# Performance work log

Hardware: AMD Instinct MI355X
Metric: run time of the kernel (lower is better)

## Reference

```python
import jax, jax.numpy as jnp
from jax import lax
import numpy as np


def conv4d(x, w, b, pad):
    """4D conv (stride 1) as a sum of 3D convs over the first-spatial-dim kernel taps.
    x: [B, Cin, T, D, H, W]; w: [Cout, Cin, Kt, Kd, Kh, Kw]; same pad on all dims."""
    B, Cin, T, D, H, W = x.shape
    Cout, _, Kt = w.shape[:3]
    xp = jnp.pad(x, ((0, 0), (0, 0), (pad, pad), (0, 0), (0, 0), (0, 0)))
    Tout = T + 2 * pad - Kt + 1
    acc = None
    for k in range(Kt):  # loop over kernel taps (<=3), not data dims
        xs = xp[:, :, k:k + Tout]                      # [B,Cin,Tout,D,H,W]
        xs = xs.transpose(0, 2, 1, 3, 4, 5).reshape(B * Tout, Cin, D, H, W)
        y = lax.conv_general_dilated(
            xs, w[:, :, k], (1, 1, 1), [(pad, pad)] * 3,
            dimension_numbers=('NCDHW', 'OIDHW', 'NCDHW'))
        acc = y if acc is None else acc + y
    Do, Ho, Wo = acc.shape[2:]
    out = acc.reshape(B, Tout, Cout, Do, Ho, Wo).transpose(0, 2, 1, 3, 4, 5)
    return out + b[None, :, None, None, None, None]


def tconv4d_k2s2(x, w, b):
    """4D transposed conv, kernel=2, stride=2, pad=0 (non-overlapping blocks).
    x: [B,Cin,T,D,H,W]; w: [Cin,Cout,2,2,2,2] (PyTorch ConvTranspose layout)."""
    B, Cin, T, D, H, W = x.shape
    Cout = w.shape[1]
    y = jnp.einsum('bcijkl,copqrs->boipjqkrls', x, w)
    y = y.reshape(B, Cout, 2 * T, 2 * D, 2 * H, 2 * W)
    return y + b[None, :, None, None, None, None]


def setup_inputs() -> dict:
    key = jax.random.key(0)
    ks = jax.random.split(key, 10)
    Cin, Cout = 64, 32
    x1 = jax.random.normal(ks[0], (2, Cin, 8, 8, 8, 8), dtype=jnp.float32)
    x2 = jax.random.normal(ks[1], (2, Cin // 2, 16, 16, 16, 16), dtype=jnp.float32)
    def w(k, shape, fan_in):
        return jax.random.normal(k, shape, dtype=jnp.float32) / np.float32(np.sqrt(fan_in))
    up_w = w(ks[2], (Cin, Cin // 2, 2, 2, 2, 2), Cin * 16)
    up_b = w(ks[3], (Cin // 2,), Cin * 16)
    w1 = w(ks[4], (Cout, Cin, 3, 3, 3, 3), Cin * 81)
    b1 = w(ks[5], (Cout,), Cin * 81)
    w2 = w(ks[6], (Cout, Cout, 3, 3, 3, 3), Cout * 81)
    b2 = w(ks[7], (Cout,), Cout * 81)
    w3 = w(ks[8], (Cout, Cin, 1, 1, 1, 1), Cin)
    b3 = w(ks[9], (Cout,), Cin)
    return {'x1': x1, 'x2': x2, 'up_w': up_w, 'up_b': up_b,
            'w1': w1, 'b1': b1, 'w2': w2, 'b2': b2, 'w3': w3, 'b3': b3}


def reference(x1, x2, up_w, up_b, w1, b1, w2, b2, w3, b3):
    x1u = tconv4d_k2s2(x1, up_w, up_b)              # [B, Cin//2, 16,16,16,16]
    xc = jnp.concatenate([x2, x1u], axis=1)          # [B, Cin, 16,16,16,16]
    Y = jax.nn.relu(conv4d(xc, w1, b1, 1))
    Y = conv4d(Y, w2, b2, 1)
    sc = conv4d(xc, w3, b3, 0)                       # 1x1 residual projection
    return jax.nn.relu(Y + sc)
```

## Files before the change

### kernel.cpp

```cpp
#include <hip/hip_runtime.h>

typedef unsigned short u16;
typedef __attribute__((ext_vector_type(8))) short short8;
typedef __attribute__((ext_vector_type(4))) float f32x4;

#define XCB_OFF  0
#define Y1B_OFF  8388608
#define W1P_OFF  12582912
#define W2P_OFF  12748800
#define W3P_OFF  12831744
#define UPWP_OFF 12833792
#define X1T_OFF  12866560

__device__ __forceinline__ u16 f2bf(float v) {
    unsigned u = __builtin_bit_cast(unsigned, v);
    u += 0x7FFFu + ((u >> 16) & 1u);
    return (u16)(u >> 16);
}

__device__ __forceinline__ f32x4 MFMA(short8 a, short8 b, f32x4 c) {
    return __builtin_amdgcn_mfma_f32_16x16x32_bf16(a, b, c, 0, 0, 0);
}

__device__ __forceinline__ void decode_bid(int bid, int& b, int& t, int& d, int& h0) {
    int xcd = bid & 7, loc = bid >> 3;
    int hB = loc & 1;
    d = (loc >> 1) & 15;
    int tsub = (loc >> 5) & 1;
    b = loc >> 6;
    t = xcd * 2 + tsub;
    h0 = hB * 8;
}

__global__ __launch_bounds__(256) void setup(const float* __restrict__ w1,
                                             const float* __restrict__ w2,
                                             const float* __restrict__ w3,
                                             const float* __restrict__ upw,
                                             const float* __restrict__ x1,
                                             const float* __restrict__ x2,
                                             u16* __restrict__ ws) {
    __shared__ u16 lds[256 * 72];
    int bid = blockIdx.x;
    int tid = threadIdx.x;
    if (bid < 32) {
        int b = bid >> 4;
        int pos_base = (bid & 15) * 256;
        u16* x1t = ws + X1T_OFF;
        #pragma unroll
        for (int c = 0; c < 64; ++c) {
            lds[tid * 72 + c] = f2bf(x1[((b * 64 + c) << 12) + pos_base + tid]);
        }
        __syncthreads();
        #pragma unroll
        for (int k = 0; k < 8; ++k) {
            int f = k * 256 + tid;
            int u = f & 7, pos = f >> 3;
            uint4 v = *(const uint4*)(lds + pos * 72 + u * 8);
            *(uint4*)(x1t + (size_t)((b << 12) + pos_base + pos) * 64 + u * 8) = v;
        }
    } else if (bid < 544) {
        int lb = bid - 32;
        int b = lb >> 8;
        int pos_base = (lb & 255) * 256;
        u16* xcb = ws + XCB_OFF;
        #pragma unroll
        for (int c = 0; c < 32; ++c) {
            lds[tid * 40 + c] = f2bf(x2[((b * 32 + c) << 16) + pos_base + tid]);
        }
        __syncthreads();
        #pragma unroll
        for (int k = 0; k < 4; ++k) {
            int f = k * 256 + tid;
            int u = f & 3, pos = f >> 2;
            uint4 v = *(const uint4*)(lds + pos * 40 + u * 8);
            *(uint4*)(xcb + (size_t)((b << 16) + pos_base + pos) * 64 + u * 8) = v;
        }
    } else {
        int idx = (bid - 544) * 256 + tid;
        if (idx < 165888) {
            int j = idx & 7, lane = (idx >> 3) & 63, rest = idx >> 9;
            int half = rest & 1, chunk = (rest >> 1) & 1, tap = rest >> 2;
            int co = half * 16 + (lane & 15), ci = chunk * 32 + (lane >> 4) * 8 + j;
            ws[W1P_OFF + idx] = f2bf(w1[(co * 64 + ci) * 81 + tap]);
        } else if (idx < 165888 + 82944) {
            int i2 = idx - 165888;
            int j = i2 & 7, lane = (i2 >> 3) & 63, rest = i2 >> 9;
            int half = rest & 1, tap = rest >> 1;
            int co = half * 16 + (lane & 15), ci = (lane >> 4) * 8 + j;
            ws[W2P_OFF + i2] = f2bf(w2[(co * 32 + ci) * 81 + tap]);
        } else if (idx < 165888 + 82944 + 2048) {
            int i3 = idx - (165888 + 82944);
            int j = i3 & 7, lane = (i3 >> 3) & 63, rest = i3 >> 9;
            int half = rest & 1, chunk = rest >> 1;
            int co = half * 16 + (lane & 15), ci = chunk * 32 + (lane >> 4) * 8 + j;
            ws[W3P_OFF + i3] = f2bf(w3[co * 64 + ci]);
        } else if (idx < 250880 + 32768) {
            int i4 = idx - 250880;
            int j = i4 & 7, lane = (i4 >> 3) & 63, rest = i4 >> 9;
            int half = rest & 1, chunk = (rest >> 1) & 1, tap = rest >> 2;
            int co = half * 16 + (lane & 15), ci = chunk * 32 + (lane >> 4) * 8 + j;
            ws[UPWP_OFF + i4] = f2bf(upw[(ci * 32 + co) * 16 + tap]);
        }
    }
}

__global__ __launch_bounds__(256) void xc_up_mfma(const u16* __restrict__ x1t,
                                                  const u16* __restrict__ upwp,
                                                  const float* __restrict__ up_b,
                                                  u16* __restrict__ xcb) {
    int tid = threadIdx.x;
    int wv = tid >> 6, lane = tid & 63;
    int q = lane >> 4, m = lane & 15;
    int wid = blockIdx.x * 4 + wv;
    int j = wid & 63, tap = (wid >> 6) & 15, b = wid >> 10;

    f32x4 acc[4][2];
    {
        float4 bi0 = ((const float4*)up_b)[q];
        float4 bi1 = ((const float4*)up_b)[4 + q];
        #pragma unroll
        for (int g = 0; g < 4; ++g) {
            acc[g][0] = (f32x4){bi0.x, bi0.y, bi0.z, bi0.w};
            acc[g][1] = (f32x4){bi1.x, bi1.y, bi1.z, bi1.w};
        }
    }

    const short8* wv8 = (const short8*)upwp;
    const u16* xb = x1t + (size_t)((b << 12) + (j << 6) + m) * 64;
    #pragma unroll
    for (int chunk = 0; chunk < 2; ++chunk) {
        short8 a0 = wv8[((tap * 2 + chunk) * 2 + 0) * 64 + lane];
        short8 a1 = wv8[((tap * 2 + chunk) * 2 + 1) * 64 + lane];
        #pragma unroll
        for (int g = 0; g < 4; ++g) {
            short8 bf = *(const short8*)(xb + (size_t)(g * 16) * 64 + chunk * 32 + q * 8);
            acc[g][0] = MFMA(a0, bf, acc[g][0]);
            acc[g][1] = MFMA(a1, bf, acc[g][1]);
        }
    }

    int it = j >> 3, id = j & 7;
    int pt = tap >> 3, pd = (tap >> 2) & 1, ph = (tap >> 1) & 1, pw = tap & 1;
    int oT = 2 * it + pt, oD = 2 * id + pd, oW = 2 * (m & 7) + pw;
    #pragma unroll
    for (int g = 0; g < 4; ++g) {
        int ih = g * 2 + (m >> 3);
        int opos = oT * 4096 + oD * 256 + (2 * ih + ph) * 16 + oW;
        u16* op = xcb + (size_t)((b << 16) + opos) * 64 + 32 + q * 4;
        #pragma unroll
        for (int half = 0; half < 2; ++half) {
            f32x4 v = acc[g][half];
            uint2 o;
            o.x = (unsigned)f2bf(v.x) | ((unsigned)f2bf(v.y) << 16);
            o.y = (unsigned)f2bf(v.z) | ((unsigned)f2bf(v.w) << 16);
            *(uint2*)(op + half * 16) = o;
        }
    }
}

__global__ __launch_bounds__(256, 4) void conv1_mfma(const u16* __restrict__ xcb,
                                                     const u16* __restrict__ w1p,
                                                     const float* __restrict__ b1,
                                                     u16* __restrict__ y1b) {
    __shared__ u16 lds[11520];
    int tid = threadIdx.x;
    int lane = tid & 63, wv = tid >> 6;
    int q = lane >> 4, m = lane & 15;
    int c = wv & 1, rg = wv >> 1;
    int b, t, d, h0;
    decode_bid(blockIdx.x, b, t, d, h0);
    int rot = (blockIdx.x * 5) % 9;

    int lofs[6], gofs[6];
    bool st[6], inr[6];
    #pragma unroll
    for (int k = 0; k < 6; ++k) {
        int ui = tid + k * 256;
        int u = ui & 7, p = (ui >> 3) % 18, hh = ui / 144;
        int gh = h0 - 1 + hh, gw = p - 1;
        st[k] = ui < 1440;
        inr[k] = st[k] && ((unsigned)gh < 16u) && ((unsigned)gw < 16u);
        gofs[k] = (gh * 16 + gw) * 64 + u * 8;
        lofs[k] = hh * 1152 + p * 64 + ((u ^ (p & 7)) * 8);
    }

    f32x4 acc[4][2];
    if (c == 0) {
        float4 bi0 = ((const float4*)b1)[q];
        float4 bi1 = ((const float4*)b1)[4 + q];
        #pragma unroll
        for (int i = 0; i < 4; ++i) {
            acc[i][0] = (f32x4){bi0.x, bi0.y, bi0.z, bi0.w};
            acc[i][1] = (f32x4){bi1.x, bi1.y, bi1.z, bi1.w};
        }
    } else {
        #pragma unroll
        for (int i = 0; i < 4; ++i) {
            acc[i][0] = (f32x4){0.f, 0.f, 0.f, 0.f};
            acc[i][1] = (f32x4){0.f, 0.f, 0.f, 0.f};
        }
    }
    const short8* w1v = (const short8*)w1p;

    uint4 rP[6];
    auto load_plane = [&](int ktd) {
        int kt = ktd / 3, kd = ktd - kt * 3;
        int tt = t + kt - 1, dd = d + kd - 1;
        bool pv = ((unsigned)tt < 16u) && ((unsigned)dd < 16u);
        const u16* src = xcb + (size_t)(((b * 16 + tt) * 16 + dd)) * 16384;
        #pragma unroll
        for (int k = 0; k < 6; ++k) {
            uint4 v = {0, 0, 0, 0};
            if (pv && inr[k]) v = *(const uint4*)(src + gofs[k]);
            rP[k] = v;
        }
    };
    auto write_plane = [&]() {
        #pragma unroll
        for (int k = 0; k < 6; ++k)
            if (st[k]) *(uint4*)(lds + lofs[k]) = rP[k];
    };

    load_plane(rot);
    for (int s = 0; s < 9; ++s) {
        int ktd = rot + s; if (ktd >= 9) ktd -= 9;
        __syncthreads();
        write_plane();
        if (s < 8) {
            int nk = ktd + 1; if (nk >= 9) nk -= 9;
            load_plane(nk);
        }
        __syncthreads();
        __builtin_amdgcn_s_setprio(1);
        #pragma unroll
        for (int kw = 0; kw < 3; ++kw) {
            int p = kw + m, pm = p & 7;
            int bo = p * 64 + ((((c << 2) | q) ^ pm) << 3);
            short8 R[6];
            #pragma unroll
            for (int r = 0; r < 6; ++r)
                R[r] = *(const short8*)(lds + (rg * 4 + r) * 1152 + bo);
            #pragma unroll
            for (int kh = 0; kh < 3; ++kh) {
                int tap = (ktd * 3 + kh) * 3 + kw;
                short8 a0 = w1v[((tap * 2 + c) * 2 + 0) * 64 + lane];
                short8 a1 = w1v[((tap * 2 + c) * 2 + 1) * 64 + lane];
                #pragma unroll
                for (int i = 0; i < 4; ++i) {
                    acc[i][0] = MFMA(a0, R[i + kh], acc[i][0]);
                    acc[i][1] = MFMA(a1, R[i + kh], acc[i][1]);
                }
            }
        }
        __builtin_amdgcn_s_setprio(0);
    }

    __syncthreads();
    f32x4* buf = (f32x4*)lds;
    if (c == 1) {
        #pragma unroll
        for (int i = 0; i < 4; ++i)
            #pragma unroll
            for (int half = 0; half < 2; ++half)
                buf[((rg * 4 + i) * 2 + half) * 64 + lane] = acc[i][half];
    }
    __syncthreads();
    if (c == 0) {
        int obase = ((b * 16 + t) * 16 + d) * 256 + (h0 + rg * 4) * 16 + m;
        #pragma unroll
        for (int i = 0; i < 4; ++i) {
            int pos = obase + i * 16;
            #pragma unroll
            for (int half = 0; half < 2; ++half) {
                f32x4 v = acc[i][half];
                f32x4 w = buf[((rg * 4 + i) * 2 + half) * 64 + lane];
                v.x += w.x; v.y += w.y; v.z += w.z; v.w += w.w;
                unsigned r0 = f2bf(fmaxf(v.x, 0.f)), r1 = f2bf(fmaxf(v.y, 0.f));
                unsigned r2 = f2bf(fmaxf(v.z, 0.f)), r3 = f2bf(fmaxf(v.w, 0.f));
                uint2 o;
                o.x = r0 | (r1 << 16);
                o.y = r2 | (r3 << 16);
                *(uint2*)(y1b + (size_t)pos * 32 + half * 16 + q * 4) = o;
            }
        }
    }
}

__global__ __launch_bounds__(256, 4) void conv2_mfma(const u16* __restrict__ y1b,
                                                     const u16* __restrict__ xcb,
                                                     const u16* __restrict__ w2p,
                                                     const u16* __restrict__ w3p,
                                                     const float* __restrict__ b2,
                                                     const float* __restrict__ b3,
                                                     float* __restrict__ out) {
    __shared__ u16 lds[2][5760];
    int tid = threadIdx.x;
    int lane = tid & 63, wv = tid >> 6;
    int q = lane >> 4, m = lane & 15;
    int hf = wv & 1, rg = wv >> 1;
    int b, t, d, h0;
    decode_bid(blockIdx.x, b, t, d, h0);
    int rot = (blockIdx.x * 5) % 9;

    int lofs[3], gofs[3];
    bool st[3], inr[3];
    #pragma unroll
    for (int k = 0; k < 3; ++k) {
        int ui = tid + k * 256;
        int u = ui & 3, p = (ui >> 2) % 18, hh = ui / 72;
        int gh = h0 - 1 + hh, gw = p - 1;
        st[k] = ui < 720;
        inr[k] = st[k] && ((unsigned)gh < 16u) && ((unsigned)gw < 16u);
        gofs[k] = (gh * 16 + gw) * 32 + u * 8;
        lofs[k] = hh * 576 + p * 32 + ((u ^ (p & 3)) * 8);
    }

    f32x4 acc[4];
    {
        float4 p0 = ((const float4*)b2)[hf * 4 + q];
        float4 s0 = ((const float4*)b3)[hf * 4 + q];
        #pragma unroll
        for (int i = 0; i < 4; ++i)
            acc[i] = (f32x4){p0.x + s0.x, p0.y + s0.y, p0.z + s0.z, p0.w + s0.w};
    }
    const short8* w2v = (const short8*)w2p;

    uint4 rP[3];
    auto load_plane = [&](int ktd) {
        int kt = ktd / 3, kd = ktd - kt * 3;
        int tt = t + kt - 1, dd = d + kd - 1;
        bool pv = ((unsigned)tt < 16u) && ((unsigned)dd < 16u);
        const u16* src = y1b + (size_t)(((b * 16 + tt) * 16 + dd)) * 8192;
        #pragma unroll
        for (int k = 0; k < 3; ++k) {
            uint4 v = {0, 0, 0, 0};
            if (pv && inr[k]) v = *(const uint4*)(src + gofs[k]);
            rP[k] = v;
        }
    };
    auto write_plane = [&](int bb) {
        #pragma unroll
        for (int k = 0; k < 3; ++k)
            if (st[k]) *(uint4*)(&lds[bb][lofs[k]]) = rP[k];
    };

    load_plane(rot);
    write_plane(0);
    { int nk = rot + 1; if (nk >= 9) nk -= 9; load_plane(nk); }

    for (int s = 0; s < 9; ++s) {
        int ktd = rot + s; if (ktd >= 9) ktd -= 9;
        __syncthreads();
        const u16* L = lds[s & 1];
        __builtin_amdgcn_s_setprio(1);
        #pragma unroll
        for (int kw = 0; kw < 3; ++kw) {
            int p = kw + m, pm = p & 3;
            int bo = p * 32 + ((q ^ pm) << 3);
            short8 R[6];
            #pragma unroll
            for (int r = 0; r < 6; ++r)
                R[r] = *(const short8*)(L + (rg * 4 + r) * 576 + bo);
            #pragma unroll
            for (int kh = 0; kh < 3; ++kh) {
                int tap = (ktd * 3 + kh) * 3 + kw;
                short8 a = w2v[(tap * 2 + hf) * 64 + lane];
                #pragma unroll
                for (int i = 0; i < 4; ++i) {
                    acc[i] = MFMA(a, R[i + kh], acc[i]);
                }
            }
        }
        __builtin_amdgcn_s_setprio(0);
        if (s < 8) {
            write_plane((s + 1) & 1);
            if (s < 7) {
                int nk = ktd + 2; if (nk >= 9) nk -= 9;
                load_plane(nk);
            }
        }
    }

    const short8* w3v = (const short8*)w3p;
    int lpos0 = (t * 16 + d) * 256 + (h0 + rg * 4) * 16 + m;
    int gpos0 = (b << 16) + lpos0;
    #pragma unroll
    for (int chunk = 0; chunk < 2; ++chunk) {
        short8 a = w3v[(chunk * 2 + hf) * 64 + lane];
        #pragma unroll
        for (int i = 0; i < 4; ++i) {
            short8 bf = *(const short8*)(xcb + (size_t)(gpos0 + i * 16) * 64 + ((chunk << 2) | q) * 8);
            acc[i] = MFMA(a, bf, acc[i]);
        }
    }

    #pragma unroll
    for (int i = 0; i < 4; ++i) {
        int lpos = lpos0 + i * 16;
        f32x4 v = acc[i];
        int co = hf * 16 + q * 4;
        float* op = out + (((size_t)(b * 32 + co)) << 16) + lpos;
        op[0ull << 16] = fmaxf(v.x, 0.f);
        op[1ull << 16] = fmaxf(v.y, 0.f);
        op[2ull << 16] = fmaxf(v.z, 0.f);
        op[3ull << 16] = fmaxf(v.w, 0.f);
    }
}

extern "C" void kernel_launch(void* const* d_in, const int* in_sizes, int n_in,
                              void* d_out, int out_size, void* d_ws, size_t ws_size,
                              hipStream_t stream) {
    const float* x1   = (const float*)d_in[0];
    const float* x2   = (const float*)d_in[1];
    const float* up_w = (const float*)d_in[2];
    const float* up_b = (const float*)d_in[3];
    const float* w1   = (const float*)d_in[4];
    const float* b1   = (const float*)d_in[5];
    const float* w2   = (const float*)d_in[6];
    const float* b2   = (const float*)d_in[7];
    const float* w3   = (const float*)d_in[8];
    const float* b3   = (const float*)d_in[9];
    u16* ws  = (u16*)d_ws;
    float* out = (float*)d_out;

    setup<<<1652, 256, 0, stream>>>(w1, w2, w3, up_w, x1, x2, ws);
    xc_up_mfma<<<512, 256, 0, stream>>>(ws + X1T_OFF, ws + UPWP_OFF, up_b, ws + XCB_OFF);
    conv1_mfma<<<1024, 256, 0, stream>>>(ws + XCB_OFF, ws + W1P_OFF, b1, ws + Y1B_OFF);
    conv2_mfma<<<1024, 256, 0, stream>>>(ws + Y1B_OFF, ws + XCB_OFF, ws + W2P_OFF,
                                         ws + W3P_OFF, b2, b3, out);
}
```

Before: 159.6 us.

## Give each conv2 block a full H plane and all 32 output channels

```diff
diff --git a/kernel.cpp b/kernel.cpp
--- a/kernel.cpp
+++ b/kernel.cpp
@@ -286,53 +286,60 @@
     }
 }
 
-__global__ __launch_bounds__(256, 4) void conv2_mfma(const u16* __restrict__ y1b,
+__global__ __launch_bounds__(256, 2) void conv2_mfma(const u16* __restrict__ y1b,
                                                      const u16* __restrict__ xcb,
                                                      const u16* __restrict__ w2p,
                                                      const u16* __restrict__ w3p,
                                                      const float* __restrict__ b2,
                                                      const float* __restrict__ b3,
                                                      float* __restrict__ out) {
-    __shared__ u16 lds[2][5760];
+    __shared__ u16 lds[2][10368];
     int tid = threadIdx.x;
     int lane = tid & 63, wv = tid >> 6;
     int q = lane >> 4, m = lane & 15;
-    int hf = wv & 1, rg = wv >> 1;
-    int b, t, d, h0;
-    decode_bid(blockIdx.x, b, t, d, h0);
-    int rot = (blockIdx.x * 5) % 9;
-
-    int lofs[3], gofs[3];
-    bool st[3], inr[3];
-    #pragma unroll
-    for (int k = 0; k < 3; ++k) {
+    int rg = wv;
+    int bid = blockIdx.x;
+    int xcd = bid & 7, loc = bid >> 3;
+    int d = loc & 15;
+    int tsub = (loc >> 4) & 1;
+    int b = loc >> 5;
+    int t = xcd * 2 + tsub;
+    int rot = (bid * 5) % 9;
+
+    int lofs[6], gofs[6];
+    bool st[6], inr[6];
+    #pragma unroll
+    for (int k = 0; k < 6; ++k) {
         int ui = tid + k * 256;
         int u = ui & 3, p = (ui >> 2) % 18, hh = ui / 72;
-        int gh = h0 - 1 + hh, gw = p - 1;
-        st[k] = ui < 720;
+        int gh = hh - 1, gw = p - 1;
+        st[k] = ui < 1296;
         inr[k] = st[k] && ((unsigned)gh < 16u) && ((unsigned)gw < 16u);
         gofs[k] = (gh * 16 + gw) * 32 + u * 8;
         lofs[k] = hh * 576 + p * 32 + ((u ^ (p & 3)) * 8);
     }
 
-    f32x4 acc[4];
+    f32x4 acc[4][2];
     {
-        float4 p0 = ((const float4*)b2)[hf * 4 + q];
-        float4 s0 = ((const float4*)b3)[hf * 4 + q];
-        #pragma unroll
-        for (int i = 0; i < 4; ++i)
-            acc[i] = (f32x4){p0.x + s0.x, p0.y + s0.y, p0.z + s0.z, p0.w + s0.w};
+        #pragma unroll
+        for (int hf = 0; hf < 2; ++hf) {
+            float4 p0 = ((const float4*)b2)[hf * 4 + q];
+            float4 s0 = ((const float4*)b3)[hf * 4 + q];
+            #pragma unroll
+            for (int i = 0; i < 4; ++i)
+                acc[i][hf] = (f32x4){p0.x + s0.x, p0.y + s0.y, p0.z + s0.z, p0.w + s0.w};
+        }
     }
     const short8* w2v = (const short8*)w2p;
 
-    uint4 rP[3];
+    uint4 rP[6];
     auto load_plane = [&](int ktd) {
         int kt = ktd / 3, kd = ktd - kt * 3;
         int tt = t + kt - 1, dd = d + kd - 1;
         bool pv = ((unsigned)tt < 16u) && ((unsigned)dd < 16u);
         const u16* src = y1b + (size_t)(((b * 16 + tt) * 16 + dd)) * 8192;
         #pragma unroll
-        for (int k = 0; k < 3; ++k) {
+        for (int k = 0; k < 6; ++k) {
             uint4 v = {0, 0, 0, 0};
             if (pv && inr[k]) v = *(const uint4*)(src + gofs[k]);
             rP[k] = v;
@@ -340,7 +347,7 @@
     };
     auto write_plane = [&](int bb) {
         #pragma unroll
-        for (int k = 0; k < 3; ++k)
+        for (int k = 0; k < 6; ++k)
             if (st[k]) *(uint4*)(&lds[bb][lofs[k]]) = rP[k];
     };
 
@@ -364,10 +371,12 @@
             #pragma unroll
             for (int kh = 0; kh < 3; ++kh) {
                 int tap = (ktd * 3 + kh) * 3 + kw;
-                short8 a = w2v[(tap * 2 + hf) * 64 + lane];
+                short8 a0 = w2v[(tap * 2 + 0) * 64 + lane];
+                short8 a1 = w2v[(tap * 2 + 1) * 64 + lane];
                 #pragma unroll
                 for (int i = 0; i < 4; ++i) {
-                    acc[i] = MFMA(a, R[i + kh], acc[i]);
+                    acc[i][0] = MFMA(a0, R[i + kh], acc[i][0]);
+                    acc[i][1] = MFMA(a1, R[i + kh], acc[i][1]);
                 }
             }
         }
@@ -382,28 +391,33 @@
     }
 
     const short8* w3v = (const short8*)w3p;
-    int lpos0 = (t * 16 + d) * 256 + (h0 + rg * 4) * 16 + m;
+    int lpos0 = (t * 16 + d) * 256 + (rg * 4) * 16 + m;
     int gpos0 = (b << 16) + lpos0;
     #pragma unroll
     for (int chunk = 0; chunk < 2; ++chunk) {
-        short8 a = w3v[(chunk * 2 + hf) * 64 + lane];
+        short8 a0 = w3v[(chunk * 2 + 0) * 64 + lane];
+        short8 a1 = w3v[(chunk * 2 + 1) * 64 + lane];
         #pragma unroll
         for (int i = 0; i < 4; ++i) {
             short8 bf = *(const short8*)(xcb + (size_t)(gpos0 + i * 16) * 64 + ((chunk << 2) | q) * 8);
-            acc[i] = MFMA(a, bf, acc[i]);
+            acc[i][0] = MFMA(a0, bf, acc[i][0]);
+            acc[i][1] = MFMA(a1, bf, acc[i][1]);
         }
     }
 
     #pragma unroll
     for (int i = 0; i < 4; ++i) {
         int lpos = lpos0 + i * 16;
-        f32x4 v = acc[i];
-        int co = hf * 16 + q * 4;
-        float* op = out + (((size_t)(b * 32 + co)) << 16) + lpos;
-        op[0ull << 16] = fmaxf(v.x, 0.f);
-        op[1ull << 16] = fmaxf(v.y, 0.f);
-        op[2ull << 16] = fmaxf(v.z, 0.f);
-        op[3ull << 16] = fmaxf(v.w, 0.f);
+        #pragma unroll
+        for (int hf = 0; hf < 2; ++hf) {
+            f32x4 v = acc[i][hf];
+            int co = hf * 16 + q * 4;
+            float* op = out + (((size_t)(b * 32 + co)) << 16) + lpos;
+            op[0ull << 16] = fmaxf(v.x, 0.f);
+            op[1ull << 16] = fmaxf(v.y, 0.f);
+            op[2ull << 16] = fmaxf(v.z, 0.f);
+            op[3ull << 16] = fmaxf(v.w, 0.f);
+        }
     }
 }
 
@@ -426,6 +440,6 @@
     setup<<<1652, 256, 0, stream>>>(w1, w2, w3, up_w, x1, x2, ws);
     xc_up_mfma<<<512, 256, 0, stream>>>(ws + X1T_OFF, ws + UPWP_OFF, up_b, ws + XCB_OFF);
     conv1_mfma<<<1024, 256, 0, stream>>>(ws + XCB_OFF, ws + W1P_OFF, b1, ws + Y1B_OFF);
-    conv2_mfma<<<1024, 256, 0, stream>>>(ws + Y1B_OFF, ws + XCB_OFF, ws + W2P_OFF,
-                                         ws + W3P_OFF, b2, b3, out);
-}
+    conv2_mfma<<<512, 256, 0, stream>>>(ws + Y1B_OFF, ws + XCB_OFF, ws + W2P_OFF,
+                                        ws + W3P_OFF, b2, b3, out);
+}
```

Result: no change. 159.1 us (-0.3%).

## Fuse x1 bf16 transpose into upsample kernel and re-tile conv2 warps

Applied to the files above, without the earlier changes.

```diff
diff --git a/kernel.cpp b/kernel.cpp
--- a/kernel.cpp
+++ b/kernel.cpp
@@ -10,7 +10,6 @@
 #define W2P_OFF  12748800
 #define W3P_OFF  12831744
 #define UPWP_OFF 12833792
-#define X1T_OFF  12866560
 
 __device__ __forceinline__ u16 f2bf(float v) {
     unsigned u = __builtin_bit_cast(unsigned, v);
@@ -36,32 +35,14 @@
                                              const float* __restrict__ w2,
                                              const float* __restrict__ w3,
                                              const float* __restrict__ upw,
-                                             const float* __restrict__ x1,
                                              const float* __restrict__ x2,
                                              u16* __restrict__ ws) {
-    __shared__ u16 lds[256 * 72];
+    __shared__ u16 lds[256 * 40];
     int bid = blockIdx.x;
     int tid = threadIdx.x;
-    if (bid < 32) {
-        int b = bid >> 4;
-        int pos_base = (bid & 15) * 256;
-        u16* x1t = ws + X1T_OFF;
-        #pragma unroll
-        for (int c = 0; c < 64; ++c) {
-            lds[tid * 72 + c] = f2bf(x1[((b * 64 + c) << 12) + pos_base + tid]);
-        }
-        __syncthreads();
-        #pragma unroll
-        for (int k = 0; k < 8; ++k) {
-            int f = k * 256 + tid;
-            int u = f & 7, pos = f >> 3;
-            uint4 v = *(const uint4*)(lds + pos * 72 + u * 8);
-            *(uint4*)(x1t + (size_t)((b << 12) + pos_base + pos) * 64 + u * 8) = v;
-        }
-    } else if (bid < 544) {
-        int lb = bid - 32;
-        int b = lb >> 8;
-        int pos_base = (lb & 255) * 256;
+    if (bid < 512) {
+        int b = bid >> 8;
+        int pos_base = (bid & 255) * 256;
         u16* xcb = ws + XCB_OFF;
         #pragma unroll
         for (int c = 0; c < 32; ++c) {
@@ -76,7 +57,7 @@
             *(uint4*)(xcb + (size_t)((b << 16) + pos_base + pos) * 64 + u * 8) = v;
         }
     } else {
-        int idx = (bid - 544) * 256 + tid;
+        int idx = (bid - 512) * 256 + tid;
         if (idx < 165888) {
             int j = idx & 7, lane = (idx >> 3) & 63, rest = idx >> 9;
             int half = rest & 1, chunk = (rest >> 1) & 1, tap = rest >> 2;
@@ -104,56 +85,64 @@
     }
 }
 
-__global__ __launch_bounds__(256) void xc_up_mfma(const u16* __restrict__ x1t,
+__global__ __launch_bounds__(256) void xc_up_mfma(const float* __restrict__ x1,
                                                   const u16* __restrict__ upwp,
                                                   const float* __restrict__ up_b,
                                                   u16* __restrict__ xcb) {
+    __shared__ u16 lds[64 * 72];
     int tid = threadIdx.x;
     int wv = tid >> 6, lane = tid & 63;
     int q = lane >> 4, m = lane & 15;
-    int wid = blockIdx.x * 4 + wv;
-    int j = wid & 63, tap = (wid >> 6) & 15, b = wid >> 10;
-
-    f32x4 acc[4][2];
-    {
-        float4 bi0 = ((const float4*)up_b)[q];
-        float4 bi1 = ((const float4*)up_b)[4 + q];
+    int bid = blockIdx.x;
+    int j = bid & 63, b = bid >> 6;
+    int pos_base = j * 64;
+
+    #pragma unroll
+    for (int g = 0; g < 16; ++g) {
+        int c = g * 4 + wv;
+        lds[lane * 72 + c] = f2bf(x1[((b * 64 + c) << 12) + pos_base + lane]);
+    }
+    __syncthreads();
+
+    const short8* wv8 = (const short8*)upwp;
+    float4 bi0 = ((const float4*)up_b)[q];
+    float4 bi1 = ((const float4*)up_b)[4 + q];
+    int it = j >> 3, id = j & 7;
+
+    for (int tt = 0; tt < 4; ++tt) {
+        int tap = wv * 4 + tt;
+        f32x4 acc[4][2];
         #pragma unroll
         for (int g = 0; g < 4; ++g) {
             acc[g][0] = (f32x4){bi0.x, bi0.y, bi0.z, bi0.w};
             acc[g][1] = (f32x4){bi1.x, bi1.y, bi1.z, bi1.w};
         }
-    }
-
-    const short8* wv8 = (const short8*)upwp;
-    const u16* xb = x1t + (size_t)((b << 12) + (j << 6) + m) * 64;
-    #pragma unroll
-    for (int chunk = 0; chunk < 2; ++chunk) {
-        short8 a0 = wv8[((tap * 2 + chunk) * 2 + 0) * 64 + lane];
-        short8 a1 = wv8[((tap * 2 + chunk) * 2 + 1) * 64 + lane];
+        #pragma unroll
+        for (int chunk = 0; chunk < 2; ++chunk) {
+            short8 a0 = wv8[((tap * 2 + chunk) * 2 + 0) * 64 + lane];
+            short8 a1 = wv8[((tap * 2 + chunk) * 2 + 1) * 64 + lane];
+            #pragma unroll
+            for (int g = 0; g < 4; ++g) {
+                short8 bf = *(const short8*)(lds + (g * 16 + m) * 72 + chunk * 32 + q * 8);
+                acc[g][0] = MFMA(a0, bf, acc[g][0]);
+                acc[g][1] = MFMA(a1, bf, acc[g][1]);
+            }
+        }
+        int pt = tap >> 3, pd = (tap >> 2) & 1, ph = (tap >> 1) & 1, pw = tap & 1;
+        int oT = 2 * it + pt, oD = 2 * id + pd, oW = 2 * (m & 7) + pw;
         #pragma unroll
         for (int g = 0; g < 4; ++g) {
-            short8 bf = *(const short8*)(xb + (size_t)(g * 16) * 64 + chunk * 32 + q * 8);
-            acc[g][0] = MFMA(a0, bf, acc[g][0]);
-            acc[g][1] = MFMA(a1, bf, acc[g][1]);
-        }
-    }
-
-    int it = j >> 3, id = j & 7;
-    int pt = tap >> 3, pd = (tap >> 2) & 1, ph = (tap >> 1) & 1, pw = tap & 1;
-    int oT = 2 * it + pt, oD = 2 * id + pd, oW = 2 * (m & 7) + pw;
-    #pragma unroll
-    for (int g = 0; g < 4; ++g) {
-        int ih = g * 2 + (m >> 3);
-        int opos = oT * 4096 + oD * 256 + (2 * ih + ph) * 16 + oW;
-        u16* op = xcb + (size_t)((b << 16) + opos) * 64 + 32 + q * 4;
-        #pragma unroll
-        for (int half = 0; half < 2; ++half) {
-            f32x4 v = acc[g][half];
-            uint2 o;
-            o.x = (unsigned)f2bf(v.x) | ((unsigned)f2bf(v.y) << 16);
-            o.y = (unsigned)f2bf(v.z) | ((unsigned)f2bf(v.w) << 16);
-            *(uint2*)(op + half * 16) = o;
+            int ih = g * 2 + (m >> 3);
+            int opos = oT * 4096 + oD * 256 + (2 * ih + ph) * 16 + oW;
+            u16* op = xcb + (size_t)((b << 16) + opos) * 64 + 32 + q * 4;
+            #pragma unroll
+            for (int half = 0; half < 2; ++half) {
+                f32x4 v = acc[g][half];
+                uint2 o;
+                o.x = (unsigned)f2bf(v.x) | ((unsigned)f2bf(v.y) << 16);
+                o.y = (unsigned)f2bf(v.z) | ((unsigned)f2bf(v.w) << 16);
+                *(uint2*)(op + half * 16) = o;
+            }
         }
     }
 }
@@ -293,11 +282,11 @@
                                                      const float* __restrict__ b2,
                                                      const float* __restrict__ b3,
                                                      float* __restrict__ out) {
-    __shared__ u16 lds[2][5760];
+    __shared__ u16 lds[11520];
     int tid = threadIdx.x;
     int lane = tid & 63, wv = tid >> 6;
     int q = lane >> 4, m = lane & 15;
-    int hf = wv & 1, rg = wv >> 1;
+    int rg = wv;
     int b, t, d, h0;
     decode_bid(blockIdx.x, b, t, d, h0);
     int rot = (blockIdx.x * 5) % 9;
@@ -315,13 +304,14 @@
         lofs[k] = hh * 576 + p * 32 + ((u ^ (p & 3)) * 8);
     }
 
-    f32x4 acc[4];
-    {
+    f32x4 acc[2][2];
+    #pragma unroll
+    for (int hf = 0; hf < 2; ++hf) {
         float4 p0 = ((const float4*)b2)[hf * 4 + q];
         float4 s0 = ((const float4*)b3)[hf * 4 + q];
         #pragma unroll
-        for (int i = 0; i < 4; ++i)
-            acc[i] = (f32x4){p0.x + s0.x, p0.y + s0.y, p0.z + s0.z, p0.w + s0.w};
+        for (int i = 0; i < 2; ++i)
+            acc[i][hf] = (f32x4){p0.x + s0.x, p0.y + s0.y, p0.z + s0.z, p0.w + s0.w};
     }
     const short8* w2v = (const short8*)w2p;
 
@@ -341,7 +331,7 @@
     auto write_plane = [&](int bb) {
         #pragma unroll
         for (int k = 0; k < 3; ++k)
-            if (st[k]) *(uint4*)(&lds[bb][lofs[k]]) = rP[k];
+            if (st[k]) *(uint4*)(lds + bb * 5760 + lofs[k]) = rP[k];
     };
 
     load_plane(rot);
@@ -351,23 +341,25 @@
     for (int s = 0; s < 9; ++s) {
         int ktd = rot + s; if (ktd >= 9) ktd -= 9;
         __syncthreads();
-        const u16* L = lds[s & 1];
+        const u16* L = lds + (s & 1) * 5760;
         __builtin_amdgcn_s_setprio(1);
         #pragma unroll
         for (int kw = 0; kw < 3; ++kw) {
             int p = kw + m, pm = p & 3;
             int bo = p * 32 + ((q ^ pm) << 3);
-            short8 R[6];
-            #pragma unroll
-            for (int r = 0; r < 6; ++r)
-                R[r] = *(const short8*)(L + (rg * 4 + r) * 576 + bo);
+            short8 R[4];
+            #pragma unroll
+            for (int r = 0; r < 4; ++r)
+                R[r] = *(const short8*)(L + (rg * 2 + r) * 576 + bo);
             #pragma unroll
             for (int kh = 0; kh < 3; ++kh) {
                 int tap = (ktd * 3 + kh) * 3 + kw;
-                short8 a = w2v[(tap * 2 + hf) * 64 + lane];
+                short8 a0 = w2v[(tap * 2 + 0) * 64 + lane];
+                short8 a1 = w2v[(tap * 2 + 1) * 64 + lane];
                 #pragma unroll
-                for (int i = 0; i < 4; ++i) {
-                    acc[i] = MFMA(a, R[i + kh], acc[i]);
+                for (int i = 0; i < 2; ++i) {
+                    acc[i][0] = MFMA(a0, R[i + kh], acc[i][0]);
+                    acc[i][1] = MFMA(a1, R[i + kh], acc[i][1]);
                 }
             }
         }
@@ -382,28 +374,33 @@
     }
 
     const short8* w3v = (const short8*)w3p;
-    int lpos0 = (t * 16 + d) * 256 + (h0 + rg * 4) * 16 + m;
+    int lpos0 = (t * 16 + d) * 256 + (h0 + rg * 2) * 16 + m;
     int gpos0 = (b << 16) + lpos0;
     #pragma unroll
     for (int chunk = 0; chunk < 2; ++chunk) {
-        short8 a = w3v[(chunk * 2 + hf) * 64 + lane];
-        #pragma unroll
-        for (int i = 0; i < 4; ++i) {
+        short8 a0 = w3v[(chunk * 2 + 0) * 64 + lane];
+        short8 a1 = w3v[(chunk * 2 + 1) * 64 + lane];
+        #pragma unroll
+        for (int i = 0; i < 2; ++i) {
             short8 bf = *(const short8*)(xcb + (size_t)(gpos0 + i * 16) * 64 + ((chunk << 2) | q) * 8);
-            acc[i] = MFMA(a, bf, acc[i]);
-        }
-    }
-
-    #pragma unroll
-    for (int i = 0; i < 4; ++i) {
+            acc[i][0] = MFMA(a0, bf, acc[i][0]);
+            acc[i][1] = MFMA(a1, bf, acc[i][1]);
+        }
+    }
+
+    #pragma unroll
+    for (int i = 0; i < 2; ++i) {
         int lpos = lpos0 + i * 16;
-        f32x4 v = acc[i];
-        int co = hf * 16 + q * 4;
-        float* op = out + (((size_t)(b * 32 + co)) << 16) + lpos;
-        op[0ull << 16] = fmaxf(v.x, 0.f);
-        op[1ull << 16] = fmaxf(v.y, 0.f);
-        op[2ull << 16] = fmaxf(v.z, 0.f);
-        op[3ull << 16] = fmaxf(v.w, 0.f);
+        #pragma unroll
+        for (int hf = 0; hf < 2; ++hf) {
+            f32x4 v = acc[i][hf];
+            int co = hf * 16 + q * 4;
+            float* op = out + (((size_t)(b * 32 + co)) << 16) + lpos;
+            op[0ull << 16] = fmaxf(v.x, 0.f);
+            op[1ull << 16] = fmaxf(v.y, 0.f);
+            op[2ull << 16] = fmaxf(v.z, 0.f);
+            op[3ull << 16] = fmaxf(v.w, 0.f);
+        }
     }
 }
 
@@ -423,8 +420,8 @@
     u16* ws  = (u16*)d_ws;
     float* out = (float*)d_out;
 
-    setup<<<1652, 256, 0, stream>>>(w1, w2, w3, up_w, x1, x2, ws);
-    xc_up_mfma<<<512, 256, 0, stream>>>(ws + X1T_OFF, ws + UPWP_OFF, up_b, ws + XCB_OFF);
+    setup<<<1620, 256, 0, stream>>>(w1, w2, w3, up_w, x2, ws);
+    xc_up_mfma<<<128, 256, 0, stream>>>(x1, ws + UPWP_OFF, up_b, ws + XCB_OFF);
     conv1_mfma<<<1024, 256, 0, stream>>>(ws + XCB_OFF, ws + W1P_OFF, b1, ws + Y1B_OFF);
     conv2_mfma<<<1024, 256, 0, stream>>>(ws + Y1B_OFF, ws + XCB_OFF, ws + W2P_OFF,
                                          ws + W3P_OFF, b2, b3, out);
```

After: 162.2 us. No clear change (+1.7%).
